# Optimization experiments

Hardware: AMD Instinct MI355X
Metric: run time of the kernel (lower is better)

Reference implementation:

```python
import jax, jax.numpy as jnp
import numpy as np

T, B, DG, DH, S = 48, 96, 192, 384, 3
LAM, ETA = 0.9, 0.5
LN_EPS = 1e-5

def layernorm(x, g, b):
    m = jnp.mean(x, axis=-1, keepdims=True)
    v = jnp.var(x, axis=-1, keepdims=True)
    return (x - m) * jax.lax.rsqrt(v + LN_EPS) * g + b

def setup_inputs() -> dict:
    key = jax.random.key(0)
    k0, k1, k2, k3 = jax.random.split(key, 4)
    z_seq = jax.random.normal(k0, (T, B, DG), jnp.float32)
    # kaiming-uniform-ish / xavier-ish scaling for realism
    W_h = jax.random.normal(k1, (DH, DH), jnp.float32) * (2.0 / DH) ** 0.5
    W_g = jax.random.normal(k2, (DH, DG), jnp.float32) * (1.0 / DG) ** 0.5
    b_h = jnp.zeros((DH,), jnp.float32)
    ln_g = jnp.ones((DH,), jnp.float32)
    ln_b = jnp.zeros((DH,), jnp.float32)
    alpha_fw = jax.random.uniform(k3, (1,), jnp.float32)  # cfg.alpha_fw (learned scalar)
    return dict(z_seq=z_seq, W_h=W_h, W_g=W_g, b_h=b_h, ln_g=ln_g, ln_b=ln_b, alpha_fw=alpha_fw)

def reference(z_seq, W_h, W_g, b_h, ln_g, ln_b, alpha_fw):
    # compute_k(): curvature of cosine gate
    k = jnp.where(alpha_fw >= 0,
                  1.0 + jax.nn.softplus(alpha_fw),
                  1.0 / (1.0 + jax.nn.softplus(-alpha_fw)))  # shape (1,)

    def step(carry, z_t):
        h, A = carry                                   # h: [B,DH], A: [B,DH,DH]
        h_base = h @ W_h.T + z_t @ W_g.T + b_h          # [B,DH]
        h_s = jax.nn.relu(layernorm(h_base, ln_g, ln_b))
        # inner fast-weight settling loop with cosine-similarity gate
        for _ in range(S):
            Ah = jnp.einsum('bij,bj->bi', A, h_s)       # bmm(A, h)
            dot = jnp.sum(h_s * Ah, axis=-1, keepdims=True)
            n1 = jnp.maximum(jnp.linalg.norm(h_s, axis=-1, keepdims=True), 1e-6)
            n2 = jnp.maximum(jnp.linalg.norm(Ah, axis=-1, keepdims=True), 1e-6)
            R = jnp.clip(dot / (n1 * n2), 0.0, 1.0)
            a = 1.0 - (1.0 - R) ** k                    # alpha_dyn, [B,1]
            h_s = jax.nn.relu(layernorm((1.0 - a * a) * h_base + a * Ah, ln_g, ln_b))
        h = h_s
        # Hebbian fast-weight update: A <- lambda*A + eta * h h^T
        A = LAM * A + ETA * jnp.einsum('bi,bj->bij', h, h)
        return (h, A), None

    Bn, Dh = z_seq.shape[1], W_h.shape[0]
    h0 = jnp.zeros((Bn, Dh), z_seq.dtype)
    A0 = jnp.zeros((Bn, Dh, Dh), z_seq.dtype)
    (h, A), _ = jax.lax.scan(step, (h0, A0), z_seq[:-1])

    # final (query) step: no gating, no A update, h_s = relu(LN(h_base + A h_s))
    z_t = z_seq[-1]
    h_base = h @ W_h.T + z_t @ W_g.T + b_h
    h = jax.nn.relu(layernorm(h_base, ln_g, ln_b))
    for _ in range(S):
        Ah = jnp.einsum('bij,bj->bi', A, h)
        h = jax.nn.relu(layernorm(h_base + Ah, ln_g, ln_b))
    return h
```

## Files before the change

kernel.cpp:

```cpp
#include <hip/hip_runtime.h>
#include <math.h>

#define TT    48
#define BB    96
#define DG    192
#define DH    384
#define NSTEP 47
#define SETI  3
#define NT    512
#define NWAVE 8
#define NOW   6
#define NG    32
#define RPG   12
#define LWROWS 192
#define LWSTR  97
#define PREPNT 768

typedef unsigned short ushort_t;
typedef float f32x2 __attribute__((ext_vector_type(2)));

template <int CTRL, int RM>
__device__ __forceinline__ float dppadd(float acc, float x) {
  int t = __builtin_amdgcn_update_dpp(0, __float_as_int(x), CTRL, RM, 0xF, false);
  return acc + __int_as_float(t);
}

__device__ __forceinline__ float row16_sum(float v) {
  v = dppadd<0x128, 0xF>(v, v);
  v = dppadd<0x124, 0xF>(v, v);
  v = dppadd<0x122, 0xF>(v, v);
  v = dppadd<0x121, 0xF>(v, v);
  return v;
}

__device__ __forceinline__ float wave_sum63(float v) {
  v = row16_sum(v);
  v = dppadd<0x142, 0xA>(v, v);
  v = dppadd<0x143, 0xC>(v, v);
  return v;
}

__device__ __forceinline__ float blo(unsigned u) {
  return __uint_as_float(u << 16);
}
__device__ __forceinline__ float bhi(unsigned u) {
  return __uint_as_float(u & 0xFFFF0000u);
}
__device__ __forceinline__ f32x2 pkfma(f32x2 a, f32x2 b, f32x2 c) {
  return __builtin_elementwise_fma(a, b, c);
}

__device__ __forceinline__ float rowdot(const uint2* w, const f32x2 (&h2)[12]) {
  f32x2 a0 = {0.f, 0.f}, a1 = {0.f, 0.f};
#pragma unroll
  for (int c = 0; c < 6; ++c) {
    uint2 u = w[c];
    a0 = pkfma(f32x2{blo(u.x), bhi(u.x)}, h2[2 * c], a0);
    a1 = pkfma(f32x2{blo(u.y), bhi(u.y)}, h2[2 * c + 1], a1);
  }
  return row16_sum((a0.x + a1.x) + (a0.y + a1.y));
}

__device__ __forceinline__ void matvec_full(
    const uint2* __restrict__ lwh, const ushort_t* __restrict__ Wh_b,
    const float* __restrict__ hs, const float* __restrict__ gzs,
    float* __restrict__ hbs, float& s1, float& s2,
    int g, int lane16, bool with_h)
{
  float rs[RPG];
  if (with_h) {
    const uint2* wsrc = (const uint2*)Wh_b;
    uint2 uw0[12];
#pragma unroll
    for (int pp = 0; pp < 2; ++pp)
#pragma unroll
      for (int c = 0; c < 6; ++c)
        uw0[pp * 6 + c] =
            wsrc[(size_t)(g + NG * (6 + pp)) * (DH / 4) + lane16 + 16 * c];
    f32x2 h2[12];
    const float4* h4 = (const float4*)hs;
#pragma unroll
    for (int c = 0; c < 6; ++c) {
      float4 hh = h4[lane16 + 16 * c];
      h2[2 * c]     = f32x2{hh.x, hh.y};
      h2[2 * c + 1] = f32x2{hh.z, hh.w};
    }
    uint2 uw1[12];
#pragma unroll
    for (int pp = 0; pp < 2; ++pp)
#pragma unroll
      for (int c = 0; c < 6; ++c)
        uw1[pp * 6 + c] =
            wsrc[(size_t)(g + NG * (8 + pp)) * (DH / 4) + lane16 + 16 * c];
#pragma unroll
    for (int p = 0; p < 6; ++p) {
      const int r = g + NG * p;
      f32x2 a0 = {0.f, 0.f}, a1 = {0.f, 0.f};
#pragma unroll
      for (int c = 0; c < 6; ++c) {
        uint2 u = lwh[r * LWSTR + lane16 + 16 * c];
        a0 = pkfma(f32x2{blo(u.x), bhi(u.x)}, h2[2 * c], a0);
        a1 = pkfma(f32x2{blo(u.y), bhi(u.y)}, h2[2 * c + 1], a1);
      }
      rs[p] = row16_sum((a0.x + a1.x) + (a0.y + a1.y));
    }
    rs[6] = rowdot(uw0, h2);
    rs[7] = rowdot(uw0 + 6, h2);
    uint2 uw2[12];
#pragma unroll
    for (int pp = 0; pp < 2; ++pp)
#pragma unroll
      for (int c = 0; c < 6; ++c)
        uw2[pp * 6 + c] =
            wsrc[(size_t)(g + NG * (10 + pp)) * (DH / 4) + lane16 + 16 * c];
    rs[8] = rowdot(uw1, h2);
    rs[9] = rowdot(uw1 + 6, h2);
    rs[10] = rowdot(uw2, h2);
    rs[11] = rowdot(uw2 + 6, h2);
  } else {
#pragma unroll
    for (int p = 0; p < RPG; ++p) rs[p] = 0.f;
  }
  if (lane16 == 0) {
#pragma unroll
    for (int p = 0; p < RPG; ++p) {
      const int r = g + NG * p;
      float vv = rs[p] + gzs[r];
      hbs[r] = vv;
      s1 += vv;
      s2 += vv * vv;
    }
  }
}

__device__ __forceinline__ void matvec_ref(
    const float* __restrict__ Wh_f, const float* __restrict__ Wg_f,
    const float* __restrict__ hs, const float* __restrict__ zsh,
    const float (&bias)[RPG], float* __restrict__ hbs,
    float& s1, float& s2, int g, int lane16, bool with_h)
{
  f32x2 h2[12];
  if (with_h) {
    const float4* h4 = (const float4*)hs;
#pragma unroll
    for (int c = 0; c < 6; ++c) {
      float4 hh = h4[lane16 + 16 * c];
      h2[2 * c]     = f32x2{hh.x, hh.y};
      h2[2 * c + 1] = f32x2{hh.z, hh.w};
    }
  }
  float4 zz[3];
  const float4* z4 = (const float4*)zsh;
#pragma unroll
  for (int c = 0; c < 3; ++c) zz[c] = z4[lane16 + 16 * c];
#pragma unroll 2
  for (int p = 0; p < RPG; ++p) {
    const int r = g + NG * p;
    f32x2 a0 = {0.f, 0.f}, a1 = {0.f, 0.f};
    const float4* wg = (const float4*)Wg_f + (size_t)r * (DG / 4);
#pragma unroll
    for (int c = 0; c < 3; ++c) {
      float4 w = wg[lane16 + 16 * c];
      a0 = pkfma(f32x2{w.x, w.y}, f32x2{zz[c].x, zz[c].y}, a0);
      a1 = pkfma(f32x2{w.z, w.w}, f32x2{zz[c].z, zz[c].w}, a1);
    }
    if (with_h) {
      const float4* wh = (const float4*)Wh_f + (size_t)r * (DH / 4);
#pragma unroll
      for (int c = 0; c < 6; ++c) {
        float4 w = wh[lane16 + 16 * c];
        a0 = pkfma(f32x2{w.x, w.y}, h2[2 * c], a0);
        a1 = pkfma(f32x2{w.z, w.w}, h2[2 * c + 1], a1);
      }
    }
    float acc = row16_sum((a0.x + a1.x) + (a0.y + a1.y));
    if (lane16 == 0) {
      float vv = acc + bias[p];
      hbs[r] = vv;
      s1 += vv;
      s2 += vv * vv;
    }
  }
}

template <bool FULL>
__global__ __launch_bounds__(NT, 2) void fw_rnn_kernel(
    const float* __restrict__ z_seq,
    const float* __restrict__ Wh_f,
    const float* __restrict__ Wg_f,
    const ushort_t* __restrict__ Wh_b,
    const float* __restrict__ gz,
    const float* __restrict__ b_h,
    const float* __restrict__ ln_g,
    const float* __restrict__ ln_b,
    const float* __restrict__ alpha_fw,
    float* __restrict__ out)
{
  __shared__ __align__(16) uint2 lwh[LWROWS * LWSTR];
  __shared__ __align__(16) float hs[DH];
  __shared__ __align__(16) float hbs[DH];
  __shared__ __align__(16) float gzs[DH];
  __shared__ __align__(16) float zsh[DG];
  __shared__ float wlam[NSTEP];
  __shared__ __align__(16) float carr[48];
  __shared__ __align__(16) float redA[NWAVE * 2];
  __shared__ __align__(16) float redB[2][32];

  const int tid    = threadIdx.x;
  const int b      = blockIdx.x;
  const int lane   = tid & 63, wv = tid >> 6;
  const int g      = tid >> 4, lane16 = tid & 15;
  const bool owner = (tid < DH);
  const bool zst   = (!FULL) && (tid >= DH) && (tid < DH + DG / 4);

  if (FULL) {
    const uint2* src = (const uint2*)Wh_b;
    for (int i = tid; i < LWROWS * 96; i += NT) {
      int row = i / 96, col = i - 96 * (i / 96);
      lwh[row * LWSTR + col] = src[(size_t)row * 96 + col];
    }
  }

  float bias[RPG];
#pragma unroll
  for (int p = 0; p < RPG; ++p) bias[p] = 0.f;
  if (!FULL && lane16 == 0) {
#pragma unroll
    for (int p = 0; p < RPG; ++p) bias[p] = b_h[g + NG * p];
  }
  float g_i = 0.f, be_i = 0.f;
  if (owner) { g_i = ln_g[tid]; be_i = ln_b[tid]; }

  const float af   = alpha_fw[0];
  const float kcur = (af >= 0.f) ? (1.f + log1pf(expf(af)))
                                 : (1.f / (1.f + log1pf(expf(-af))));
  const float invD = 1.0f / (float)DH;

  float hcol[48];
#pragma unroll
  for (int q = 0; q < 48; ++q) hcol[q] = 0.f;
  float4 hregA[6], hregB[6];
#pragma unroll
  for (int c = 0; c < 6; ++c) {
    hregA[c] = float4{0.f, 0.f, 0.f, 0.f};
    hregB[c] = float4{0.f, 0.f, 0.f, 0.f};
  }

  if (FULL && tid < DH / 4)
    ((float4*)gzs)[tid] = ((const float4*)(gz + (size_t)b * DH))[tid];
  if (!FULL && tid < DG / 4)
    ((float4*)zsh)[tid] = ((const float4*)(z_seq + (size_t)b * DG))[tid];
  if (tid < 48) carr[tid] = 0.f;
  if (tid < 2) { redB[tid][30] = 0.f; redB[tid][31] = 0.f; }
  __syncthreads();

  float Shb = 0.f, Shb2 = 0.f;

  for (int t = 0; t < NSTEP; ++t) {
    float4 gzn = {0.f, 0.f, 0.f, 0.f};
    if (FULL && tid < DH / 4)
      gzn = ((const float4*)(gz + ((size_t)(t + 1) * BB + b) * DH))[tid];

    float s1 = 0.f, s2 = 0.f;
    if (FULL)
      matvec_full(lwh, Wh_b, hs, gzs, hbs, s1, s2, g, lane16, t > 0);
    else
      matvec_ref(Wh_f, Wg_f, hs, zsh, bias, hbs, s1, s2, g, lane16, t > 0);

    if (t > 0) {
      if (g == t - 1) {
#pragma unroll
        for (int c = 0; c < 6; ++c) hregA[c] = ((const float4*)hs)[lane16 + 16 * c];
      }
      if (g + NG == t - 1) {
#pragma unroll
        for (int c = 0; c < 6; ++c) hregB[c] = ((const float4*)hs)[lane16 + 16 * c];
      }
    }
    {
      float v0 = wave_sum63(s1);
      float v1 = wave_sum63(s2);
      if (lane == 63) { redA[wv * 2] = v0; redA[wv * 2 + 1] = v1; }
    }
    __syncthreads();

    float hb = 0.f, hsv = 0.f;
    if (owner) {
      float S1 = 0.f, S2 = 0.f;
      const float4* ra4 = (const float4*)redA;
#pragma unroll
      for (int q = 0; q < 4; ++q) {
        float4 ch = ra4[q];
        S1 += ch.x + ch.z;
        S2 += ch.y + ch.w;
      }
      Shb = S1; Shb2 = S2;
      hb = hbs[tid];
      float m   = S1 * invD;
      float var = S2 * invD - m * m;
      hsv = fmaxf((hb - m) * rsqrtf(var + 1e-5f) * g_i + be_i, 0.f);
      hs[tid] = hsv;
    }
    if (t == 0) {
      if (owner) hcol[0] = hsv;
      if (tid == 0) wlam[0] = 0.5f;
      if (FULL && tid < DH / 4) ((float4*)gzs)[tid] = gzn;
      if (zst)
        ((float4*)zsh)[tid - DH] =
            ((const float4*)(z_seq + ((size_t)1 * BB + b) * DG))[tid - DH];
      __syncthreads();
      continue;
    }
    __syncthreads();

    float4 znext;
    if (zst)
      znext = ((const float4*)(z_seq + ((size_t)(t + 1) * BB + b) * DG))[tid - DH];

    for (int s = 0; s < SETI; ++s) {
      if (g < t) {
        float4 ss[6];
        const float4* s4 = (const float4*)hs;
#pragma unroll
        for (int c = 0; c < 6; ++c) ss[c] = s4[lane16 + 16 * c];
        {
          f32x2 p0 = {0.f, 0.f}, p1 = {0.f, 0.f};
#pragma unroll
          for (int c = 0; c < 6; ++c) {
            p0 = pkfma(f32x2{hregA[c].x, hregA[c].y}, f32x2{ss[c].x, ss[c].y}, p0);
            p1 = pkfma(f32x2{hregA[c].z, hregA[c].w}, f32x2{ss[c].z, ss[c].w}, p1);
          }
          float p = row16_sum((p0.x + p1.x) + (p0.y + p1.y));
          if (lane16 == 0) carr[g] = p * wlam[g];
        }
        if (g + NG < t) {
          f32x2 p0 = {0.f, 0.f}, p1 = {0.f, 0.f};
#pragma unroll
          for (int c = 0; c < 6; ++c) {
            p0 = pkfma(f32x2{hregB[c].x, hregB[c].y}, f32x2{ss[c].x, ss[c].y}, p0);
            p1 = pkfma(f32x2{hregB[c].z, hregB[c].w}, f32x2{ss[c].z, ss[c].w}, p1);
          }
          float p = row16_sum((p0.x + p1.x) + (p0.y + p1.y));
          if (lane16 == 0) carr[g + NG] = p * wlam[g + NG];
        }
      }
      __syncthreads();

      float ah = 0.f;
      if (owner) {
        const float4* c4 = (const float4*)carr;
        float a0 = 0.f, a1 = 0.f, a2 = 0.f, a3 = 0.f;
#pragma unroll
        for (int q = 0; q < 12; ++q) {
          float4 cc = c4[q];
          a0 = fmaf(cc.x, hcol[4 * q + 0], a0);
          a1 = fmaf(cc.y, hcol[4 * q + 1], a1);
          a2 = fmaf(cc.z, hcol[4 * q + 2], a2);
          a3 = fmaf(cc.w, hcol[4 * q + 3], a3);
        }
        ah = (a0 + a2) + (a1 + a3);
        float v0 = wave_sum63(hsv * ah);
        float v1 = wave_sum63(hsv * hsv);
        float v2 = wave_sum63(ah * ah);
        float v3 = wave_sum63(hb * ah);
        float v4 = wave_sum63(ah);
        if (lane == 63) {
          float* rb = redB[s & 1];
          rb[wv * 5 + 0] = v0; rb[wv * 5 + 1] = v1; rb[wv * 5 + 2] = v2;
          rb[wv * 5 + 3] = v3; rb[wv * 5 + 4] = v4;
        }
      }
      __syncthreads();

      if (owner) {
        const float4* rb4 = (const float4*)redB[s & 1];
        float S[5] = {0.f, 0.f, 0.f, 0.f, 0.f};
#pragma unroll
        for (int q = 0; q < 8; ++q) {
          float4 ch = rb4[q];
          S[(4 * q + 0) % 5] += ch.x;
          S[(4 * q + 1) % 5] += ch.y;
          S[(4 * q + 2) % 5] += ch.z;
          S[(4 * q + 3) % 5] += ch.w;
        }
        float n1 = fmaxf(sqrtf(S[1]), 1e-6f);
        float n2 = fmaxf(sqrtf(S[2]), 1e-6f);
        float R  = fminf(fmaxf(__fdividef(S[0], n1 * n2), 0.f), 1.f);
        float a  = 1.f - __expf(kcur * __logf(1.f - R));
        float beta = 1.f - a * a;
        float mu  = (beta * Shb + a * S[4]) * invD;
        float Exx = (beta * beta * Shb2 + 2.f * beta * a * S[3] + a * a * S[2]) * invD;
        float var = Exx - mu * mu;
        float xv  = beta * hb + a * ah;
        hsv = fmaxf((xv - mu) * rsqrtf(var + 1e-5f) * g_i + be_i, 0.f);
        hs[tid] = hsv;
        if (s == SETI - 1) {
#pragma unroll
          for (int q = 0; q < 48; ++q)
            if (q == t) hcol[q] = hsv;
        }
      }
      if (s == SETI - 1) {
        if (tid < t) wlam[tid] *= 0.9f;
        else if (tid == t) wlam[tid] = 0.5f;
        if (FULL && tid < DH / 4) ((float4*)gzs)[tid] = gzn;
        if (zst) ((float4*)zsh)[tid - DH] = znext;
      }
      __syncthreads();
    }
  }

  {
    float s1 = 0.f, s2 = 0.f;
    if (FULL)
      matvec_full(lwh, Wh_b, hs, gzs, hbs, s1, s2, g, lane16, true);
    else
      matvec_ref(Wh_f, Wg_f, hs, zsh, bias, hbs, s1, s2, g, lane16, true);
    if (g + NG == NSTEP - 1) {
#pragma unroll
      for (int c = 0; c < 6; ++c) hregB[c] = ((const float4*)hs)[lane16 + 16 * c];
    }
    {
      float v0 = wave_sum63(s1);
      float v1 = wave_sum63(s2);
      if (lane == 63) { redA[wv * 2] = v0; redA[wv * 2 + 1] = v1; }
    }
    __syncthreads();

    float hb = 0.f, hv = 0.f;
    if (owner) {
      float S1 = 0.f, S2 = 0.f;
      const float4* ra4 = (const float4*)redA;
#pragma unroll
      for (int q = 0; q < 4; ++q) {
        float4 ch = ra4[q];
        S1 += ch.x + ch.z;
        S2 += ch.y + ch.w;
      }
      Shb = S1; Shb2 = S2;
      hb = hbs[tid];
      float m   = S1 * invD;
      float var = S2 * invD - m * m;
      hv = fmaxf((hb - m) * rsqrtf(var + 1e-5f) * g_i + be_i, 0.f);
      hs[tid] = hv;
    }
    __syncthreads();

    for (int s = 0; s < SETI; ++s) {
      {
        float4 ss[6];
        const float4* s4 = (const float4*)hs;
#pragma unroll
        for (int c = 0; c < 6; ++c) ss[c] = s4[lane16 + 16 * c];
        {
          f32x2 p0 = {0.f, 0.f}, p1 = {0.f, 0.f};
#pragma unroll
          for (int c = 0; c < 6; ++c) {
            p0 = pkfma(f32x2{hregA[c].x, hregA[c].y}, f32x2{ss[c].x, ss[c].y}, p0);
            p1 = pkfma(f32x2{hregA[c].z, hregA[c].w}, f32x2{ss[c].z, ss[c].w}, p1);
          }
          float p = row16_sum((p0.x + p1.x) + (p0.y + p1.y));
          if (lane16 == 0) carr[g] = p * wlam[g];
        }
        if (g + NG < NSTEP) {
          f32x2 p0 = {0.f, 0.f}, p1 = {0.f, 0.f};
#pragma unroll
          for (int c = 0; c < 6; ++c) {
            p0 = pkfma(f32x2{hregB[c].x, hregB[c].y}, f32x2{ss[c].x, ss[c].y}, p0);
            p1 = pkfma(f32x2{hregB[c].z, hregB[c].w}, f32x2{ss[c].z, ss[c].w}, p1);
          }
          float p = row16_sum((p0.x + p1.x) + (p0.y + p1.y));
          if (lane16 == 0) carr[g + NG] = p * wlam[g + NG];
        }
      }
      __syncthreads();

      float ah = 0.f;
      if (owner) {
        const float4* c4 = (const float4*)carr;
        float a0 = 0.f, a1 = 0.f, a2 = 0.f, a3 = 0.f;
#pragma unroll
        for (int q = 0; q < 12; ++q) {
          float4 cc = c4[q];
          a0 = fmaf(cc.x, hcol[4 * q + 0], a0);
          a1 = fmaf(cc.y, hcol[4 * q + 1], a1);
          a2 = fmaf(cc.z, hcol[4 * q + 2], a2);
          a3 = fmaf(cc.w, hcol[4 * q + 3], a3);
        }
        ah = (a0 + a2) + (a1 + a3);
        float v0 = wave_sum63(ah);
        float v1 = wave_sum63(ah * ah);
        float v2 = wave_sum63(hb * ah);
        if (lane == 63) {
          float* rb = redB[s & 1];
          rb[wv * 5 + 0] = v0; rb[wv * 5 + 1] = v1; rb[wv * 5 + 2] = v2;
        }
      }
      __syncthreads();

      if (owner) {
        const float4* rb4 = (const float4*)redB[s & 1];
        float S[5] = {0.f, 0.f, 0.f, 0.f, 0.f};
#pragma unroll
        for (int q = 0; q < 8; ++q) {
          float4 ch = rb4[q];
          S[(4 * q + 0) % 5] += ch.x;
          S[(4 * q + 1) % 5] += ch.y;
          S[(4 * q + 2) % 5] += ch.z;
          S[(4 * q + 3) % 5] += ch.w;
        }
        float Sx  = Shb + S[0];
        float Sxx = Shb2 + 2.f * S[2] + S[1];
        float mu  = Sx * invD;
        float var = Sxx * invD - mu * mu;
        float xv  = hb + ah;
        hv = fmaxf((xv - mu) * rsqrtf(var + 1e-5f) * g_i + be_i, 0.f);
        if (s < SETI - 1) hs[tid] = hv;
      }
      if (s < SETI - 1) __syncthreads();
    }

    if (owner) out[(size_t)b * DH + tid] = hv;
  }
}

__global__ __launch_bounds__(PREPNT) void prep_kernel(
    const float* __restrict__ z_seq, const float* __restrict__ Wg,
    const float* __restrict__ W_h, const float* __restrict__ b_h,
    ushort_t* __restrict__ Whb, float* __restrict__ gz)
{
  __shared__ __align__(16) float zsh[DG];
  const int tid = threadIdx.x, b = blockIdx.x;
  const int g = tid >> 4, lane16 = tid & 15;

  {
    int lid = (blockIdx.y * BB + blockIdx.x) * PREPNT + tid;
    if (lid < DH * DH) {
      unsigned u = __float_as_uint(W_h[lid]);
      unsigned r = (u + 0x7FFFu + ((u >> 16) & 1u)) >> 16;
      Whb[lid] = (ushort_t)r;
    }
  }

  float4 w[24];
#pragma unroll
  for (int p = 0; p < 8; ++p)
#pragma unroll
    for (int c = 0; c < 3; ++c)
      w[p * 3 + c] = ((const float4*)Wg)[(size_t)(8 * g + p) * (DG / 4) + lane16 + 16 * c];
  float4 bs0 = {0.f, 0.f, 0.f, 0.f}, bs1 = {0.f, 0.f, 0.f, 0.f};
  if (lane16 == 0) {
    bs0 = ((const float4*)b_h)[2 * g];
    bs1 = ((const float4*)b_h)[2 * g + 1];
  }
  for (int tt = 0; tt < 6; ++tt) {
    const int t = blockIdx.y * 6 + tt;
    __syncthreads();
    if (tid < DG / 4)
      ((float4*)zsh)[tid] = ((const float4*)(z_seq + ((size_t)t * BB + b) * DG))[tid];
    __syncthreads();
    float4 zz[3];
#pragma unroll
    for (int c = 0; c < 3; ++c) zz[c] = ((const float4*)zsh)[lane16 + 16 * c];
    float rs[8];
#pragma unroll
    for (int p = 0; p < 8; ++p) {
      f32x2 a0 = {0.f, 0.f}, a1 = {0.f, 0.f};
#pragma unroll
      for (int c = 0; c < 3; ++c) {
        a0 = pkfma(f32x2{w[p * 3 + c].x, w[p * 3 + c].y}, f32x2{zz[c].x, zz[c].y}, a0);
        a1 = pkfma(f32x2{w[p * 3 + c].z, w[p * 3 + c].w}, f32x2{zz[c].z, zz[c].w}, a1);
      }
      rs[p] = row16_sum((a0.x + a1.x) + (a0.y + a1.y));
    }
    if (lane16 == 0) {
      float* grow = gz + ((size_t)t * BB + b) * DH + 8 * g;
      ((float4*)grow)[0] = float4{rs[0] + bs0.x, rs[1] + bs0.y, rs[2] + bs0.z, rs[3] + bs0.w};
      ((float4*)grow)[1] = float4{rs[4] + bs1.x, rs[5] + bs1.y, rs[6] + bs1.z, rs[7] + bs1.w};
    }
  }
}

extern "C" void kernel_launch(void* const* d_in, const int* in_sizes, int n_in,
                              void* d_out, int out_size, void* d_ws, size_t ws_size,
                              hipStream_t stream) {
  const float* z_seq    = (const float*)d_in[0];
  const float* W_h      = (const float*)d_in[1];
  const float* W_g      = (const float*)d_in[2];
  const float* b_h      = (const float*)d_in[3];
  const float* ln_g     = (const float*)d_in[4];
  const float* ln_b     = (const float*)d_in[5];
  const float* alpha_fw = (const float*)d_in[6];
  float* out = (float*)d_out;

  const size_t nWh = (size_t)DH * DH;
  const size_t bf16Bytes = nWh * sizeof(ushort_t);
  const size_t gzBytes   = (size_t)TT * BB * DH * sizeof(float);

  if (ws_size >= bf16Bytes + gzBytes) {
    ushort_t* Whb = (ushort_t*)d_ws;
    float* gz = (float*)((char*)d_ws + bf16Bytes);
    prep_kernel<<<dim3(BB, 8), dim3(PREPNT), 0, stream>>>(
        z_seq, W_g, W_h, b_h, Whb, gz);
    fw_rnn_kernel<true><<<dim3(BB), dim3(NT), 0, stream>>>(
        z_seq, W_h, W_g, Whb, gz, b_h, ln_g, ln_b, alpha_fw, out);
  } else {
    fw_rnn_kernel<false><<<dim3(BB), dim3(NT), 0, stream>>>(
        z_seq, W_h, W_g, nullptr, nullptr, b_h, ln_g, ln_b, alpha_fw, out);
  }
}
```

Measured before the change: 524.9 us.

## Restructure prep kernel: fewer threads, stage 24 timesteps of z in LDS

The input-projection prep kernel now runs 2x96 blocks of 256 threads instead of 8x96 blocks of 768. Each thread covers three W_g row groups in sequence and reuses its register-held weights across 24 timesteps staged in shared memory at once, rather than syncing per timestep. The W_h bf16 conversion is spread over three elements per thread to match the smaller grid. This aims to cut repeated W_g loads and barriers, at the cost of less parallelism and longer per-block serial work.

After: 529.3 us. Within noise of the previous version (+0.8%).

```diff
diff --git a/kernel.cpp b/kernel.cpp
--- a/kernel.cpp
+++ b/kernel.cpp
@@ -14,7 +14,8 @@
 #define RPG   12
 #define LWROWS 192
 #define LWSTR  97
-#define PREPNT 768
+#define PNT   256
+#define PTT   24
 
 typedef unsigned short ushort_t;
 typedef float f32x2 __attribute__((ext_vector_type(2)));
@@ -524,59 +525,75 @@
   }
 }
 
-__global__ __launch_bounds__(PREPNT) void prep_kernel(
+__global__ __launch_bounds__(PNT) void prep_kernel(
     const float* __restrict__ z_seq, const float* __restrict__ Wg,
     const float* __restrict__ W_h, const float* __restrict__ b_h,
     ushort_t* __restrict__ Whb, float* __restrict__ gz)
 {
-  __shared__ __align__(16) float zsh[DG];
+  __shared__ __align__(16) float zsh[PTT * DG];
   const int tid = threadIdx.x, b = blockIdx.x;
+  const int t0 = blockIdx.y * PTT;
   const int g = tid >> 4, lane16 = tid & 15;
 
   {
-    int lid = (blockIdx.y * BB + blockIdx.x) * PREPNT + tid;
-    if (lid < DH * DH) {
-      unsigned u = __float_as_uint(W_h[lid]);
-      unsigned r = (u + 0x7FFFu + ((u >> 16) & 1u)) >> 16;
-      Whb[lid] = (ushort_t)r;
-    }
-  }
-
-  float4 w[24];
-#pragma unroll
-  for (int p = 0; p < 8; ++p)
-#pragma unroll
-    for (int c = 0; c < 3; ++c)
-      w[p * 3 + c] = ((const float4*)Wg)[(size_t)(8 * g + p) * (DG / 4) + lane16 + 16 * c];
-  float4 bs0 = {0.f, 0.f, 0.f, 0.f}, bs1 = {0.f, 0.f, 0.f, 0.f};
-  if (lane16 == 0) {
-    bs0 = ((const float4*)b_h)[2 * g];
-    bs1 = ((const float4*)b_h)[2 * g + 1];
-  }
-  for (int tt = 0; tt < 6; ++tt) {
-    const int t = blockIdx.y * 6 + tt;
-    __syncthreads();
-    if (tid < DG / 4)
-      ((float4*)zsh)[tid] = ((const float4*)(z_seq + ((size_t)t * BB + b) * DG))[tid];
-    __syncthreads();
-    float4 zz[3];
-#pragma unroll
-    for (int c = 0; c < 3; ++c) zz[c] = ((const float4*)zsh)[lane16 + 16 * c];
-    float rs[8];
-#pragma unroll
-    for (int p = 0; p < 8; ++p) {
-      f32x2 a0 = {0.f, 0.f}, a1 = {0.f, 0.f};
-#pragma unroll
-      for (int c = 0; c < 3; ++c) {
-        a0 = pkfma(f32x2{w[p * 3 + c].x, w[p * 3 + c].y}, f32x2{zz[c].x, zz[c].y}, a0);
-        a1 = pkfma(f32x2{w[p * 3 + c].z, w[p * 3 + c].w}, f32x2{zz[c].z, zz[c].w}, a1);
-      }
-      rs[p] = row16_sum((a0.x + a1.x) + (a0.y + a1.y));
-    }
+    int lid = ((blockIdx.y * BB + blockIdx.x) * PNT + tid) * 3;
+#pragma unroll
+    for (int k = 0; k < 3; ++k) {
+      int idx = lid + k;
+      if (idx < DH * DH) {
+        unsigned u = __float_as_uint(W_h[idx]);
+        unsigned r = (u + 0x7FFFu + ((u >> 16) & 1u)) >> 16;
+        Whb[idx] = (ushort_t)r;
+      }
+    }
+  }
+
+  for (int i = tid; i < PTT * DG / 4; i += PNT) {
+    int tt = i / (DG / 4), c = i - tt * (DG / 4);
+    ((float4*)zsh)[i] =
+        ((const float4*)(z_seq + ((size_t)(t0 + tt) * BB + b) * DG))[c];
+  }
+  __syncthreads();
+
+  for (int pp = 0; pp < 3; ++pp) {
+    const int rbase = 24 * g + 8 * pp;
+    float4 w[24];
+#pragma unroll
+    for (int j = 0; j < 8; ++j)
+#pragma unroll
+      for (int c = 0; c < 3; ++c)
+        w[j * 3 + c] =
+            ((const float4*)Wg)[(size_t)(rbase + j) * (DG / 4) + lane16 + 16 * c];
+    float4 bh0 = {0.f, 0.f, 0.f, 0.f}, bh1 = {0.f, 0.f, 0.f, 0.f};
     if (lane16 == 0) {
-      float* grow = gz + ((size_t)t * BB + b) * DH + 8 * g;
-      ((float4*)grow)[0] = float4{rs[0] + bs0.x, rs[1] + bs0.y, rs[2] + bs0.z, rs[3] + bs0.w};
-      ((float4*)grow)[1] = float4{rs[4] + bs1.x, rs[5] + bs1.y, rs[6] + bs1.z, rs[7] + bs1.w};
+      bh0 = ((const float4*)b_h)[rbase / 4];
+      bh1 = ((const float4*)b_h)[rbase / 4 + 1];
+    }
+    for (int tt = 0; tt < PTT; ++tt) {
+      float4 zz[3];
+#pragma unroll
+      for (int c = 0; c < 3; ++c)
+        zz[c] = ((const float4*)zsh)[tt * (DG / 4) + lane16 + 16 * c];
+      float rs[8];
+#pragma unroll
+      for (int j = 0; j < 8; ++j) {
+        f32x2 a0 = {0.f, 0.f}, a1 = {0.f, 0.f};
+#pragma unroll
+        for (int c = 0; c < 3; ++c) {
+          a0 = pkfma(f32x2{w[j * 3 + c].x, w[j * 3 + c].y},
+                     f32x2{zz[c].x, zz[c].y}, a0);
+          a1 = pkfma(f32x2{w[j * 3 + c].z, w[j * 3 + c].w},
+                     f32x2{zz[c].z, zz[c].w}, a1);
+        }
+        rs[j] = row16_sum((a0.x + a1.x) + (a0.y + a1.y));
+      }
+      if (lane16 == 0) {
+        float* grow = gz + ((size_t)(t0 + tt) * BB + b) * DH + rbase;
+        ((float4*)grow)[0] =
+            float4{rs[0] + bh0.x, rs[1] + bh0.y, rs[2] + bh0.z, rs[3] + bh0.w};
+        ((float4*)grow)[1] =
+            float4{rs[4] + bh1.x, rs[5] + bh1.y, rs[6] + bh1.z, rs[7] + bh1.w};
+      }
     }
   }
 }
@@ -600,7 +617,7 @@
   if (ws_size >= bf16Bytes + gzBytes) {
     ushort_t* Whb = (ushort_t*)d_ws;
     float* gz = (float*)((char*)d_ws + bf16Bytes);
-    prep_kernel<<<dim3(BB, 8), dim3(PREPNT), 0, stream>>>(
+    prep_kernel<<<dim3(BB, 2), dim3(PNT), 0, stream>>>(
         z_seq, W_g, W_h, b_h, Whb, gz);
     fw_rnn_kernel<true><<<dim3(BB), dim3(NT), 0, stream>>>(
         z_seq, W_h, W_g, Whb, gz, b_h, ln_g, ln_b, alpha_fw, out);
```
